# Performance work log

Hardware: AMD Instinct MI355X
Metric: run time of the kernel (lower is better)

## Reference

```python
import math
import jax, jax.numpy as jnp
import numpy as np

EPS = 1e-6
MAX_SCALE_LOG = math.log(100.0)

def rms_norm(x, scale, eps=EPS):
    # x * scale / rms(x), reduction over last dim
    ms = jnp.mean(jnp.square(x), axis=-1, keepdims=True)
    return x * (scale * jax.lax.rsqrt(ms + eps))

def axial_rope_theta(pos, n_heads, d_head, dtype):
    # freqs: linspace in log-space from pi to 10*pi, reshaped to [n_heads, d_head//4]
    f = np.exp(np.linspace(math.log(math.pi), math.log(10.0 * math.pi),
                           n_heads * d_head // 4 + 1)[:-1])
    freqs = jnp.asarray(f.reshape(d_head // 4, n_heads).T, dtype)  # [h, e/4]
    theta_h = pos[:, :, None, 0:1] * freqs  # [n, l, h, e/4]
    theta_w = pos[:, :, None, 1:2] * freqs  # [n, l, h, e/4]
    theta = jnp.concatenate([theta_h, theta_w], axis=-1)  # [n, l, h, e/2]
    return theta.transpose(0, 2, 1, 3)  # [n, h, l, e/2]

def apply_rotary(x, theta):
    d = theta.shape[-1]
    x1, x2, x3 = x[..., :d], x[..., d:2 * d], x[..., 2 * d:]
    cos, sin = jnp.cos(theta), jnp.sin(theta)
    return jnp.concatenate([x1 * cos - x2 * sin, x2 * cos + x1 * sin, x3], axis=-1)

def setup_inputs() -> dict:
    key = jax.random.key(0)
    ks = jax.random.split(key, 8)
    n, l, d_model, d_head = 2, 2048, 1024, 64
    n_heads = d_model // d_head
    x = jax.random.normal(ks[0], (n, l, d_model), jnp.float32)
    pos = jax.random.uniform(ks[1], (n, l, 2), jnp.float32)
    cond = jax.random.normal(ks[2], (n, 1, d_model), jnp.float32)
    # params (torch uses zero-init for w_cond/w_out; small random for a non-degenerate baseline)
    w_cond = jax.random.normal(ks[3], (d_model, d_model), jnp.float32) * 0.02
    w_qkv = jax.random.normal(ks[4], (d_model, 3 * d_model), jnp.float32) * (d_model ** -0.5)
    qk_scale = jnp.full((n_heads,), math.log(10.0), jnp.float32)
    w_out = jax.random.normal(ks[5], (d_model, d_model), jnp.float32) * 0.02
    return {"x": x, "pos": pos, "cond": cond, "w_cond": w_cond,
            "w_qkv": w_qkv, "qk_scale": qk_scale, "w_out": w_out}

def reference(x, pos, cond, w_cond, w_qkv, qk_scale, w_out):
    n, l, d_model = x.shape
    h = qk_scale.shape[0]
    e = d_model // h
    # AdaRMSNorm: scale = linear(cond) + 1
    xn = rms_norm(x, cond @ w_cond + 1.0)
    # QKV projection
    q, k, v = jnp.split(xn @ w_qkv, 3, axis=-1)
    to_heads = lambda t: t.reshape(n, l, h, e).transpose(0, 2, 1, 3)  # [n,h,l,e]
    q, k, v = to_heads(q), to_heads(k), to_heads(v)
    # QKNorm: per-head learned scale, rms over head dim
    s = jnp.exp(0.5 * jnp.minimum(qk_scale, MAX_SCALE_LOG) - 0.25 * math.log(e))
    q = rms_norm(q, s[:, None, None])
    k = rms_norm(k, s[:, None, None])
    # Axial RoPE
    theta = axial_rope_theta(pos, h, e, x.dtype)
    q = apply_rotary(q, theta)
    k = apply_rotary(k, theta)
    # SDPA (no mask)
    attn = jax.nn.softmax(jnp.einsum('nhqe,nhke->nhqk', q, k) / math.sqrt(e), axis=-1)
    o = jnp.einsum('nhqk,nhke->nhqe', attn, v)
    o = o.transpose(0, 2, 1, 3).reshape(n, l, d_model)
    return o @ w_out
```

## Files before the change

kernel.cpp:

```cpp
#include <hip/hip_runtime.h>

typedef unsigned short u16;
typedef unsigned int u32;
typedef short s16x8 __attribute__((ext_vector_type(8)));
typedef short s16x4 __attribute__((ext_vector_type(4)));
typedef float f32x4 __attribute__((ext_vector_type(4)));
typedef float f32x16 __attribute__((ext_vector_type(16)));

#define AS1 __attribute__((address_space(1)))
#define AS3 __attribute__((address_space(3)))

__device__ __forceinline__ float bf2f(u16 u) {
    union { unsigned int i; float f; } x; x.i = ((unsigned int)u) << 16; return x.f;
}
__device__ __forceinline__ u16 f2bf(float f) {
    union { float f; unsigned int i; } x; x.f = f;
    unsigned int r = (x.i + 0x7FFFu + ((x.i >> 16) & 1u)) >> 16;
    return (u16)r;
}
__device__ __forceinline__ void storeOut(u16* p, float v) { *p = f2bf(v); }
__device__ __forceinline__ void storeOut(float* p, float v) { *p = v; }
__device__ __forceinline__ float loadIn(const void* p, size_t i, int isf32) {
    return isf32 ? ((const float*)p)[i] : bf2f(((const u16*)p)[i]);
}
__device__ __forceinline__ float fexp2(float x) {
#if __has_builtin(__builtin_amdgcn_exp2f)
    return __builtin_amdgcn_exp2f(x);
#else
    return exp2f(x);
#endif
}
__device__ __forceinline__ void plswap(u32& a, u32& b) {
#if __has_builtin(__builtin_amdgcn_permlane32_swap)
    const auto r = __builtin_amdgcn_permlane32_swap(a, b, false, false);
    a = (u32)r[0]; b = (u32)r[1];
#else
    asm("v_permlane32_swap_b32 %0, %1" : "+v"(a), "+v"(b));
#endif
}

__global__ __launch_bounds__(256) void detect_dtype(const u16* __restrict__ x,
                                                    int* __restrict__ flag) {
    __shared__ int cnt[4];
    const int tid = threadIdx.x;
    int c = 0;
    #pragma unroll
    for (int i = 0; i < 4; ++i) {
        const u16 u = x[tid * 4 + i];
        const int e = (u >> 7) & 0xFF;
        c += (e >= 101 && e <= 135) ? 1 : 0;
    }
    #pragma unroll
    for (int m = 1; m < 64; m <<= 1) c += __shfl_xor(c, m, 64);
    if ((tid & 63) == 0) cnt[tid >> 6] = c;
    __syncthreads();
    if (tid == 0) {
        const int t = cnt[0] + cnt[1] + cnt[2] + cnt[3];
        *flag = (t < 800) ? 1 : 0;
    }
}

__global__ __launch_bounds__(256) void cond_gemv(const void* __restrict__ cond,
                                                 const void* __restrict__ w,
                                                 float* __restrict__ out,
                                                 const int* __restrict__ flag) {
    const int isf32 = *flag;
    const int d  = blockIdx.x * 256 + threadIdx.x;
    const int n  = blockIdx.y;
    const int k0 = blockIdx.z * 64;
    float acc = 0.f;
    #pragma unroll 8
    for (int k = 0; k < 64; ++k)
        acc += loadIn(cond, n * 1024 + k0 + k, isf32) *
               loadIn(w, (size_t)(k0 + k) * 1024 + d, isf32);
    atomicAdd(out + n * 1024 + d, acc);
}

__global__ __launch_bounds__(256) void rmsnorm_x(const void* __restrict__ x,
                                                 const float* __restrict__ scl,
                                                 u16* __restrict__ xn,
                                                 const int* __restrict__ flag) {
    const int isf32 = *flag;
    const int tok = blockIdx.x;
    const int n = tok >> 11;
    u16* orow = xn + (size_t)tok * 1024;
    const int base = threadIdx.x * 4;
    float f0, f1, f2, f3;
    if (isf32) {
        const float4 v = *(const float4*)((const float*)x + (size_t)tok * 1024 + base);
        f0 = v.x; f1 = v.y; f2 = v.z; f3 = v.w;
    } else {
        s16x4 uv = *(const s16x4*)((const u16*)x + (size_t)tok * 1024 + base);
        f0 = bf2f((u16)uv[0]); f1 = bf2f((u16)uv[1]); f2 = bf2f((u16)uv[2]); f3 = bf2f((u16)uv[3]);
    }
    float ss = f0 * f0 + f1 * f1 + f2 * f2 + f3 * f3;
    #pragma unroll
    for (int m = 1; m < 64; m <<= 1) ss += __shfl_xor(ss, m, 64);
    __shared__ float red[4];
    const int wave = threadIdx.x >> 6, lane = threadIdx.x & 63;
    if (lane == 0) red[wave] = ss;
    __syncthreads();
    float ms = (red[0] + red[1] + red[2] + red[3]) * (1.f / 1024.f);
    float rinv = rsqrtf(ms + 1e-6f);
    s16x4 ov;
    ov[0] = (short)f2bf(f0 * (scl[n * 1024 + base + 0] + 1.f) * rinv);
    ov[1] = (short)f2bf(f1 * (scl[n * 1024 + base + 1] + 1.f) * rinv);
    ov[2] = (short)f2bf(f2 * (scl[n * 1024 + base + 2] + 1.f) * rinv);
    ov[3] = (short)f2bf(f3 * (scl[n * 1024 + base + 3] + 1.f) * rinv);
    *(s16x4*)(orow + base) = ov;
}

__global__ __launch_bounds__(256) void transpose_bf(const void* __restrict__ src,
                                                    u16* __restrict__ dst, int R, int C,
                                                    const int* __restrict__ flag) {
    const int isf32 = *flag;
    __shared__ u16 t[32][33];
    const int c0 = blockIdx.x * 32, r0 = blockIdx.y * 32;
    const int tx = threadIdx.x & 31, ty = threadIdx.x >> 5;
    #pragma unroll
    for (int i = 0; i < 4; ++i)
        t[ty + i * 8][tx] = f2bf(loadIn(src, (size_t)(r0 + ty + i * 8) * C + c0 + tx, isf32));
    __syncthreads();
    #pragma unroll
    for (int i = 0; i < 4; ++i)
        dst[(size_t)(c0 + ty + i * 8) * R + r0 + tx] = t[tx][ty + i * 8];
}

template <typename OutT>
__global__ __launch_bounds__(256) void gemm_bt(const u16* __restrict__ A,
                                               const u16* __restrict__ BT,
                                               OutT* __restrict__ C, int Nn, int K) {
    __shared__ u16 As[2][128 * 32];
    __shared__ u16 Bs[2][128 * 32];
    const int tid = threadIdx.x;
    const int wave = tid >> 6, lane = tid & 63;
    const int l15 = lane & 15, quad = lane >> 4;
    const int bm0 = blockIdx.y * 128, bn0 = blockIdx.x * 128;
    const int wr = wave >> 1, wc = wave & 1;
    f32x4 acc[4][4] = {};
    const int srow = lane >> 2;
    const int g = (lane & 3) ^ (srow & 3);

    auto stageg = [&](int ck, int slot) {
        const int bk = ck * 32;
        #pragma unroll
        for (int p = 0; p < 2; ++p) {
            const int rowl = p * 64 + wave * 16 + srow;
            const u16* ga = A + (size_t)(bm0 + rowl) * K + bk + g * 8;
            u16* la = As[slot] + (p * 64 + wave * 16) * 32;
            __builtin_amdgcn_global_load_lds((const AS1 void*)ga, (AS3 void*)la, 16, 0, 0);
            const u16* gb = BT + (size_t)(bn0 + rowl) * K + bk + g * 8;
            u16* lb = Bs[slot] + (p * 64 + wave * 16) * 32;
            __builtin_amdgcn_global_load_lds((const AS1 void*)gb, (AS3 void*)lb, 16, 0, 0);
        }
    };

    const int NC = K >> 5;
    stageg(0, 0);
    for (int j = 0; j < NC; ++j) {
        if (j > 0) __builtin_amdgcn_s_barrier();
        if (j < NC - 1) {
            stageg(j + 1, (j + 1) & 1);
            asm volatile("s_waitcnt vmcnt(4)" ::: "memory");
        } else {
            asm volatile("s_waitcnt vmcnt(0)" ::: "memory");
        }
        __builtin_amdgcn_sched_barrier(0);
        __builtin_amdgcn_s_barrier();

        const u16* Ac = As[j & 1];
        const u16* Bc = Bs[j & 1];
        s16x8 af[4], bfr[4];
        #pragma unroll
        for (int mt = 0; mt < 4; ++mt) {
            const int r = wr * 64 + mt * 16 + l15;
            af[mt] = *(const s16x8*)(Ac + r * 32 + ((quad ^ (r & 3)) << 3));
        }
        #pragma unroll
        for (int nt = 0; nt < 4; ++nt) {
            const int r = wc * 64 + nt * 16 + l15;
            bfr[nt] = *(const s16x8*)(Bc + r * 32 + ((quad ^ (r & 3)) << 3));
        }
        #pragma unroll
        for (int mt = 0; mt < 4; ++mt)
            #pragma unroll
            for (int nt = 0; nt < 4; ++nt)
                acc[mt][nt] = __builtin_amdgcn_mfma_f32_16x16x32_bf16(af[mt], bfr[nt], acc[mt][nt], 0, 0, 0);
    }
    #pragma unroll
    for (int mt = 0; mt < 4; ++mt)
        #pragma unroll
        for (int nt = 0; nt < 4; ++nt)
            #pragma unroll
            for (int r = 0; r < 4; ++r) {
                const int row = bm0 + wr * 64 + mt * 16 + quad * 4 + r;
                const int col = bn0 + wc * 64 + nt * 16 + l15;
                storeOut(C + (size_t)row * Nn + col, acc[mt][nt][r]);
            }
}

template <typename OutT>
__global__ __launch_bounds__(256) void gemm_bt64(const u16* __restrict__ A,
                                                 const u16* __restrict__ BT,
                                                 OutT* __restrict__ C, int Nn, int K) {
    __shared__ u16 As[2][128 * 32];
    __shared__ u16 Bs[2][64 * 32];
    const int tid = threadIdx.x;
    const int wave = tid >> 6, lane = tid & 63;
    const int l15 = lane & 15, quad = lane >> 4;
    const int bm0 = blockIdx.y * 128, bn0 = blockIdx.x * 64;
    const int wr = wave >> 1, wc = wave & 1;
    f32x4 acc[4][2] = {};
    const int srow = lane >> 2;
    const int g = (lane & 3) ^ (srow & 3);

    auto stageg = [&](int ck, int slot) {
        const int bk = ck * 32;
        #pragma unroll
        for (int p = 0; p < 2; ++p) {
            const int rowl = p * 64 + wave * 16 + srow;
            const u16* ga = A + (size_t)(bm0 + rowl) * K + bk + g * 8;
            u16* la = As[slot] + (p * 64 + wave * 16) * 32;
            __builtin_amdgcn_global_load_lds((const AS1 void*)ga, (AS3 void*)la, 16, 0, 0);
        }
        {
            const int rowl = wave * 16 + srow;
            const u16* gb = BT + (size_t)(bn0 + rowl) * K + bk + g * 8;
            u16* lb = Bs[slot] + (wave * 16) * 32;
            __builtin_amdgcn_global_load_lds((const AS1 void*)gb, (AS3 void*)lb, 16, 0, 0);
        }
    };

    const int NC = K >> 5;
    stageg(0, 0);
    for (int j = 0; j < NC; ++j) {
        if (j > 0) __builtin_amdgcn_s_barrier();
        if (j < NC - 1) {
            stageg(j + 1, (j + 1) & 1);
            asm volatile("s_waitcnt vmcnt(3)" ::: "memory");
        } else {
            asm volatile("s_waitcnt vmcnt(0)" ::: "memory");
        }
        __builtin_amdgcn_sched_barrier(0);
        __builtin_amdgcn_s_barrier();

        const u16* Ac = As[j & 1];
        const u16* Bc = Bs[j & 1];
        s16x8 af[4], bfr[2];
        #pragma unroll
        for (int mt = 0; mt < 4; ++mt) {
            const int r = wr * 64 + mt * 16 + l15;
            af[mt] = *(const s16x8*)(Ac + r * 32 + ((quad ^ (r & 3)) << 3));
        }
        #pragma unroll
        for (int nt = 0; nt < 2; ++nt) {
            const int r = wc * 32 + nt * 16 + l15;
            bfr[nt] = *(const s16x8*)(Bc + r * 32 + ((quad ^ (r & 3)) << 3));
        }
        #pragma unroll
        for (int mt = 0; mt < 4; ++mt)
            #pragma unroll
            for (int nt = 0; nt < 2; ++nt)
                acc[mt][nt] = __builtin_amdgcn_mfma_f32_16x16x32_bf16(af[mt], bfr[nt], acc[mt][nt], 0, 0, 0);
    }
    #pragma unroll
    for (int mt = 0; mt < 4; ++mt)
        #pragma unroll
        for (int nt = 0; nt < 2; ++nt)
            #pragma unroll
            for (int r = 0; r < 4; ++r) {
                const int row = bm0 + wr * 64 + mt * 16 + quad * 4 + r;
                const int col = bn0 + wc * 32 + nt * 16 + l15;
                storeOut(C + (size_t)row * Nn + col, acc[mt][nt][r]);
            }
}

__global__ __launch_bounds__(256) void qkv_head(const u16* __restrict__ qkv,
                                                const void* __restrict__ pos,
                                                const void* __restrict__ qk_scale,
                                                u16* __restrict__ q_ws,
                                                u16* __restrict__ k_ws,
                                                u16* __restrict__ vtg,
                                                const int* __restrict__ flag) {
    const int isf32 = *flag;
    const int nh = blockIdx.y;
    const int n = nh >> 4, h = nh & 15;
    const int l0 = blockIdx.x * 64;
    const int tid = threadIdx.x;
    const int wave = tid >> 6, lane = tid & 63;

    const float qs = loadIn(qk_scale, h, isf32);
    const float s = __expf(0.5f * fminf(qs, 4.605170186f) - 1.039720771f);
    const float qmul = s * s * 0.125f * 1.44269504089f;
    const int j = lane & 31;
    const float t = (float)((j & 15) * 16 + h);
    const float freq = 3.14159265358979f * __expf(t * (2.302585093f / 256.f));
    const int pj = j >> 4;

    #pragma unroll 2
    for (int it = 0; it < 16; ++it) {
        const int l = l0 + wave * 16 + it;
        const int tok = n * 2048 + l;
        const u16* row = qkv + (size_t)tok * 3072;
        float qv = bf2f(row[h * 64 + lane]);
        float kv = bf2f(row[1024 + h * 64 + lane]);
        float q2 = qv * qv, k2 = kv * kv;
        #pragma unroll
        for (int m = 1; m < 64; m <<= 1) { q2 += __shfl_xor(q2, m, 64); k2 += __shfl_xor(k2, m, 64); }
        float qn = qv * rsqrtf(q2 * (1.f / 64.f) + 1e-6f) * qmul;
        float kn = kv * rsqrtf(k2 * (1.f / 64.f) + 1e-6f);
        const float p = loadIn(pos, tok * 2 + pj, isf32);
        const float th = p * freq;
        const float c = __cosf(th), sn = __sinf(th);
        const float pq = __shfl_xor(qn, 32, 64);
        const float pk = __shfl_xor(kn, 32, 64);
        float qr, kr;
        if (lane < 32) { qr = qn * c - pq * sn; kr = kn * c - pk * sn; }
        else           { qr = qn * c + pq * sn; kr = kn * c + pk * sn; }
        const size_t oidx = ((size_t)nh * 2048 + l) * 64 + lane;
        q_ws[oidx] = f2bf(qr);
        k_ws[oidx] = f2bf(kr);
    }

    __shared__ u16 tbuf[64][65];
    const u16* vsrc = qkv + (size_t)(n * 2048 + l0) * 3072 + 2048 + h * 64;
    #pragma unroll
    for (int it = 0; it < 16; ++it) {
        const int idx = it * 256 + tid;
        const int r = idx >> 6, c = idx & 63;
        tbuf[r][c] = vsrc[(size_t)r * 3072 + c];
    }
    __syncthreads();
    u16* dst = vtg + (size_t)nh * 131072 + l0;
    #pragma unroll
    for (int it = 0; it < 16; ++it) {
        const int idx = it * 256 + tid;
        const int er = idx >> 6, lc = idx & 63;
        dst[(size_t)er * 2048 + lc] = tbuf[lc][er];
    }
}

__global__ __launch_bounds__(1024) void attn10(const u16* __restrict__ Q,
                                               const u16* __restrict__ K,
                                               const u16* __restrict__ Vtg,
                                               u16* __restrict__ O) {
    __shared__ u16 Ks[2][256 * 64];
    __shared__ u16 Vt[2][64 * 256];
    const int nh = blockIdx.y;
    const int q0 = blockIdx.x * 256;
    const int tid = threadIdx.x;
    const int wave = tid >> 6, lane = tid & 63;
    const int wq = wave & 7, ks = wave >> 3;
    const int l31 = lane & 31, h = lane >> 5;
    const size_t hb = (size_t)nh * 2048 * 64;
    const u16* Vbase = Vtg + (size_t)nh * 131072;

    s16x8 qf[4];
    #pragma unroll
    for (int kd = 0; kd < 4; ++kd)
        qf[kd] = *(const s16x8*)(Q + hb + (size_t)(q0 + wq * 32 + l31) * 64 + kd * 16 + h * 8);

    f32x16 Oacc[2] = {};
    float lacc = 0.f;

    auto stage = [&](int ch, int slot) {
        const int kb = ch * 256;
        #pragma unroll
        for (int r = 0; r < 2; ++r) {
            const int row = r * 128 + (tid >> 3);
            const int g = (tid & 7) ^ (row & 7);
            __builtin_amdgcn_global_load_lds(
                (const AS1 void*)(K + hb + (size_t)(kb + row) * 64 + g * 8),
                (AS3 void*)(Ks[slot] + (r * 128 + wave * 8) * 64), 16, 0, 0);
        }
        #pragma unroll
        for (int r = 0; r < 2; ++r) {
            const int er = r * 32 + (tid >> 5);
            const int g2 = (lane & 31) ^ (er & 7);
            __builtin_amdgcn_global_load_lds(
                (const AS1 void*)(Vbase + (size_t)er * 2048 + kb + g2 * 8),
                (AS3 void*)(Vt[slot] + (r * 32 + wave * 2) * 256), 16, 0, 0);
        }
    };

    stage(0, 0);

    for (int j = 0; j < 8; ++j) {
        if (j > 0) __builtin_amdgcn_s_barrier();
        if (j < 7) {
            stage(j + 1, (j + 1) & 1);
            asm volatile("s_waitcnt vmcnt(4)" ::: "memory");
        } else {
            asm volatile("s_waitcnt vmcnt(0)" ::: "memory");
        }
        __builtin_amdgcn_sched_barrier(0);
        __builtin_amdgcn_s_barrier();

        const u16* Kt = Ks[j & 1];
        const u16* Vc = Vt[j & 1];

        #pragma unroll 2
        for (int t = 0; t < 4; ++t) {
            const int kt = ks * 4 + t;
            f32x16 S;
            #pragma unroll
            for (int jj = 0; jj < 16; ++jj) S[jj] = -15.f;
            const int kr = kt * 32 + l31;
            __builtin_amdgcn_s_setprio(1);
            #pragma unroll
            for (int kd = 0; kd < 4; ++kd) {
                const s16x8 kf = *(const s16x8*)(Kt + kr * 64 + ((((kd << 1) + h) ^ (kr & 7)) << 3));
                S = __builtin_amdgcn_mfma_f32_32x32x16_bf16(kf, qf[kd], S, 0, 0, 0);
            }
            __builtin_amdgcn_s_setprio(0);
            float e[16];
            #pragma unroll
            for (int jj = 0; jj < 16; ++jj) e[jj] = fexp2(S[jj]);
            float rs = 0.f;
            #pragma unroll
            for (int jj = 0; jj < 16; ++jj) rs += e[jj];
            lacc += rs;
            u32 c[8];
            #pragma unroll
            for (int jj = 0; jj < 8; ++jj)
                asm("v_cvt_pk_bf16_f32 %0, %1, %2" : "=v"(c[jj]) : "v"(e[2 * jj]), "v"(e[2 * jj + 1]));
            plswap(c[0], c[2]);
            plswap(c[1], c[3]);
            plswap(c[4], c[6]);
            plswap(c[5], c[7]);
            union { u32 u[4]; s16x8 v; } pfa, pfb;
            pfa.u[0] = c[0]; pfa.u[1] = c[1]; pfa.u[2] = c[2]; pfa.u[3] = c[3];
            pfb.u[0] = c[4]; pfb.u[1] = c[5]; pfb.u[2] = c[6]; pfb.u[3] = c[7];
            __builtin_amdgcn_s_setprio(1);
            #pragma unroll
            for (int et = 0; et < 2; ++et) {
                const int er = et * 32 + l31;
                #pragma unroll
                for (int kdp = 0; kdp < 2; ++kdp) {
                    const int ch = kt * 4 + kdp * 2 + h;
                    const s16x8 vf = *(const s16x8*)(Vc + er * 256 + ((ch ^ (er & 7)) << 3));
                    Oacc[et] = __builtin_amdgcn_mfma_f32_32x32x16_bf16(kdp ? pfb.v : pfa.v, vf, Oacc[et], 0, 0, 0);
                }
            }
            __builtin_amdgcn_s_setprio(0);
        }
    }

    __syncthreads();
    float (*Osh)[512] = (float(*)[512]) & Ks[0][0];
    float* Lsh = (float*)&Vt[0][0];
    if (ks == 1) {
        #pragma unroll
        for (int et = 0; et < 2; ++et)
            #pragma unroll
            for (int r = 0; r < 16; ++r)
                Osh[et * 16 + r][wq * 64 + lane] = Oacc[et][r];
        Lsh[wq * 64 + lane] = lacc;
    }
    __syncthreads();
    if (ks == 0) {
        #pragma unroll
        for (int et = 0; et < 2; ++et)
            #pragma unroll
            for (int r = 0; r < 16; ++r)
                Oacc[et][r] += Osh[et * 16 + r][wq * 64 + lane];
        lacc += Lsh[wq * 64 + lane];

        lacc += __shfl_xor(lacc, 32, 64);
        const float linv_l = 1.f / lacc;
        const int n = nh >> 4, hh = nh & 15;
        #pragma unroll
        for (int r = 0; r < 16; ++r) {
            const int ql = (r & 3) + 8 * (r >> 2) + 4 * h;
            const float linv = __shfl(linv_l, ql, 64);
            const int qrow = q0 + wq * 32 + ql;
            #pragma unroll
            for (int et = 0; et < 2; ++et)
                O[((size_t)n * 2048 + qrow) * 1024 + hh * 64 + et * 32 + l31] = f2bf(Oacc[et][r] * linv);
        }
    }
}

extern "C" void kernel_launch(void* const* d_in, const int* in_sizes, int n_in,
                              void* d_out, int out_size, void* d_ws, size_t ws_size,
                              hipStream_t stream) {
    const void* x        = d_in[0];
    const void* pos      = d_in[1];
    const void* cond     = d_in[2];
    const void* w_cond   = d_in[3];
    const void* w_qkv    = d_in[4];
    const void* qk_scale = d_in[5];
    const void* w_out    = d_in[6];

    char* ws = (char*)d_ws;
    constexpr size_t OFS_SCALE = 0;
    constexpr size_t OFS_FLAG  = 8192;
    constexpr size_t OFS_XN    = 16384;
    constexpr size_t OFS_WQKVT = OFS_XN    + 8388608;
    constexpr size_t OFS_WOUTT = OFS_WQKVT + 6291456;
    constexpr size_t OFS_QKV   = OFS_WOUTT + 2097152;
    constexpr size_t OFS_Q     = OFS_QKV   + 25165824;
    constexpr size_t OFS_K     = OFS_Q     + 8388608;
    constexpr size_t OFS_VT    = OFS_K     + 8388608;
    constexpr size_t OFS_O     = OFS_VT    + 8388608;

    float* scale = (float*)(ws + OFS_SCALE);
    int*   flag  = (int*)(ws + OFS_FLAG);
    u16* xn    = (u16*)(ws + OFS_XN);
    u16* wqkvT = (u16*)(ws + OFS_WQKVT);
    u16* woutT = (u16*)(ws + OFS_WOUTT);
    u16* qkv   = (u16*)(ws + OFS_QKV);
    u16* qws   = (u16*)(ws + OFS_Q);
    u16* kws   = (u16*)(ws + OFS_K);
    u16* vtg   = (u16*)(ws + OFS_VT);
    u16* ows   = (u16*)(ws + OFS_O);

    detect_dtype<<<dim3(1), 256, 0, stream>>>((const u16*)x, flag);
    hipMemsetAsync(scale, 0, 2 * 1024 * sizeof(float), stream);
    cond_gemv<<<dim3(4, 2, 16), 256, 0, stream>>>(cond, w_cond, scale, flag);
    rmsnorm_x<<<dim3(4096), 256, 0, stream>>>(x, scale, xn, flag);
    transpose_bf<<<dim3(96, 32), 256, 0, stream>>>(w_qkv, wqkvT, 1024, 3072, flag);
    transpose_bf<<<dim3(32, 32), 256, 0, stream>>>(w_out, woutT, 1024, 1024, flag);
    gemm_bt<u16><<<dim3(24, 32), 256, 0, stream>>>(xn, wqkvT, qkv, 3072, 1024);
    qkv_head<<<dim3(32, 32), 256, 0, stream>>>(qkv, pos, qk_scale, qws, kws, vtg, flag);
    attn10<<<dim3(8, 32), 1024, 0, stream>>>(qws, kws, vtg, ows);
    gemm_bt64<float><<<dim3(16, 32), 256, 0, stream>>>(ows, woutT, (float*)d_out, 1024, 1024);
}
```

Baseline: 222.2 us.

## Fuse QK norm, RoPE and V transpose into QKV GEMM epilogue; merge transposes

Moves the per-head QK RMS norm, axial RoPE and the V transpose from a separate qkv_head kernel into the epilogue of the QKV GEMM. Each wave's 64-column tile maps to one head, so the norm is reduced with 16-lane shuffles and RoPE is applied in registers before writing Q and K. V tiles go through shared memory and are written transposed. This removes the round trip of the 24 MB QKV intermediate and one launch, and the two weight transposes are merged into one launch. The cost is a heavier epilogue with scattered 2-byte stores for Q and K, plus a larger shared buffer.

```diff
diff --git a/kernel.cpp b/kernel.cpp
--- a/kernel.cpp
+++ b/kernel.cpp
@@ -110,12 +110,18 @@
     *(s16x4*)(orow + base) = ov;
 }
 
-__global__ __launch_bounds__(256) void transpose_bf(const void* __restrict__ src,
-                                                    u16* __restrict__ dst, int R, int C,
-                                                    const int* __restrict__ flag) {
+__global__ __launch_bounds__(256) void transpose_both(const void* __restrict__ src_qkv,
+                                                      u16* __restrict__ dst_qkv,
+                                                      const void* __restrict__ src_out,
+                                                      u16* __restrict__ dst_out,
+                                                      const int* __restrict__ flag) {
     const int isf32 = *flag;
     __shared__ u16 t[32][33];
-    const int c0 = blockIdx.x * 32, r0 = blockIdx.y * 32;
+    const void* src; u16* dst; int C, c0;
+    const int R = 1024;
+    if (blockIdx.x < 96) { src = src_qkv; dst = dst_qkv; C = 3072; c0 = blockIdx.x * 32; }
+    else                 { src = src_out; dst = dst_out; C = 1024; c0 = (blockIdx.x - 96) * 32; }
+    const int r0 = blockIdx.y * 32;
     const int tx = threadIdx.x & 31, ty = threadIdx.x >> 5;
     #pragma unroll
     for (int i = 0; i < 4; ++i)
@@ -126,12 +132,18 @@
         dst[(size_t)(c0 + ty + i * 8) * R + r0 + tx] = t[tx][ty + i * 8];
 }
 
-template <typename OutT>
-__global__ __launch_bounds__(256) void gemm_bt(const u16* __restrict__ A,
-                                               const u16* __restrict__ BT,
-                                               OutT* __restrict__ C, int Nn, int K) {
-    __shared__ u16 As[2][128 * 32];
-    __shared__ u16 Bs[2][128 * 32];
+__global__ __launch_bounds__(256) void gemm_qkv(const u16* __restrict__ A,
+                                                const u16* __restrict__ BT,
+                                                const void* __restrict__ pos,
+                                                const void* __restrict__ qk_scale,
+                                                u16* __restrict__ qws,
+                                                u16* __restrict__ kws,
+                                                u16* __restrict__ vtg,
+                                                const int* __restrict__ flag) {
+    constexpr int K = 1024;
+    __shared__ u16 sbuf[128 * 136];
+    u16* As = sbuf;
+    u16* Bs = sbuf + 8192;
     const int tid = threadIdx.x;
     const int wave = tid >> 6, lane = tid & 63;
     const int l15 = lane & 15, quad = lane >> 4;
@@ -147,10 +159,10 @@
         for (int p = 0; p < 2; ++p) {
             const int rowl = p * 64 + wave * 16 + srow;
             const u16* ga = A + (size_t)(bm0 + rowl) * K + bk + g * 8;
-            u16* la = As[slot] + (p * 64 + wave * 16) * 32;
+            u16* la = As + slot * 4096 + (p * 64 + wave * 16) * 32;
             __builtin_amdgcn_global_load_lds((const AS1 void*)ga, (AS3 void*)la, 16, 0, 0);
             const u16* gb = BT + (size_t)(bn0 + rowl) * K + bk + g * 8;
-            u16* lb = Bs[slot] + (p * 64 + wave * 16) * 32;
+            u16* lb = Bs + slot * 4096 + (p * 64 + wave * 16) * 32;
             __builtin_amdgcn_global_load_lds((const AS1 void*)gb, (AS3 void*)lb, 16, 0, 0);
         }
     };
@@ -168,8 +180,8 @@
         __builtin_amdgcn_sched_barrier(0);
         __builtin_amdgcn_s_barrier();
 
-        const u16* Ac = As[j & 1];
-        const u16* Bc = Bs[j & 1];
+        const u16* Ac = As + (j & 1) * 4096;
+        const u16* Bc = Bs + (j & 1) * 4096;
         s16x8 af[4], bfr[4];
         #pragma unroll
         for (int mt = 0; mt < 4; ++mt) {
@@ -187,16 +199,68 @@
             for (int nt = 0; nt < 4; ++nt)
                 acc[mt][nt] = __builtin_amdgcn_mfma_f32_16x16x32_bf16(af[mt], bfr[nt], acc[mt][nt], 0, 0, 0);
     }
-    #pragma unroll
-    for (int mt = 0; mt < 4; ++mt)
-        #pragma unroll
-        for (int nt = 0; nt < 4; ++nt)
-            #pragma unroll
-            for (int r = 0; r < 4; ++r) {
-                const int row = bm0 + wr * 64 + mt * 16 + quad * 4 + r;
-                const int col = bn0 + wc * 64 + nt * 16 + l15;
-                storeOut(C + (size_t)row * Nn + col, acc[mt][nt][r]);
+
+    const int isf32 = *flag;
+    const int bx = blockIdx.x;
+    const int rowbase = bm0 + wr * 64;
+    const int n = rowbase >> 11;
+    const int colw = bn0 + wc * 64;
+
+    if (bx < 16) {
+        const int isq = (bx < 8);
+        const int hh = (colw >> 6) & 15;
+        float mul = 1.f;
+        if (isq) {
+            const float qs = loadIn(qk_scale, hh, isf32);
+            const float s = __expf(0.5f * fminf(qs, 4.605170186f) - 1.039720771f);
+            mul = s * s * 0.125f * 1.44269504089f;
+        }
+        const float t = (float)(l15 * 16 + hh);
+        const float freq = 3.14159265358979f * __expf(t * (2.302585093f / 256.f));
+        u16* dstb = (isq ? qws : kws) + (size_t)(n * 16 + hh) * 2048 * 64;
+        #pragma unroll
+        for (int mt = 0; mt < 4; ++mt)
+            #pragma unroll
+            for (int rr = 0; rr < 4; ++rr) {
+                const int row = rowbase + mt * 16 + quad * 4 + rr;
+                const int l = row & 2047;
+                float s2 = acc[mt][0][rr] * acc[mt][0][rr] + acc[mt][1][rr] * acc[mt][1][rr]
+                         + acc[mt][2][rr] * acc[mt][2][rr] + acc[mt][3][rr] * acc[mt][3][rr];
+                #pragma unroll
+                for (int m = 1; m < 16; m <<= 1) s2 += __shfl_xor(s2, m, 16);
+                const float sc = rsqrtf(s2 * (1.f / 64.f) + 1e-6f) * mul;
+                const float p0 = loadIn(pos, (size_t)row * 2 + 0, isf32);
+                const float p1 = loadIn(pos, (size_t)row * 2 + 1, isf32);
+                const float c0 = __cosf(p0 * freq), sn0 = __sinf(p0 * freq);
+                const float c1 = __cosf(p1 * freq), sn1 = __sinf(p1 * freq);
+                const float a0 = acc[mt][0][rr] * sc, a1 = acc[mt][1][rr] * sc;
+                const float a2 = acc[mt][2][rr] * sc, a3 = acc[mt][3][rr] * sc;
+                u16* d = dstb + (size_t)l * 64 + l15;
+                d[0]  = f2bf(a0 * c0 - a2 * sn0);
+                d[16] = f2bf(a1 * c1 - a3 * sn1);
+                d[32] = f2bf(a2 * c0 + a0 * sn0);
+                d[48] = f2bf(a3 * c1 + a1 * sn1);
             }
+    } else {
+        __syncthreads();
+        #pragma unroll
+        for (int mt = 0; mt < 4; ++mt)
+            #pragma unroll
+            for (int nt = 0; nt < 4; ++nt)
+                #pragma unroll
+                for (int rr = 0; rr < 4; ++rr)
+                    sbuf[(wc * 64 + nt * 16 + l15) * 136 + (wr * 64 + mt * 16 + quad * 4 + rr)]
+                        = f2bf(acc[mt][nt][rr]);
+        __syncthreads();
+        const int ec = tid >> 1, half = tid & 1;
+        const int vcol = bn0 + ec - 2048;
+        const int hh = vcol >> 6, e = vcol & 63;
+        const int lbase = (bm0 & 2047) + half * 64;
+        u16* d = vtg + ((size_t)((bm0 >> 11) * 16 + hh) * 64 + e) * 2048 + lbase;
+        #pragma unroll
+        for (int i = 0; i < 8; ++i)
+            *(s16x8*)(d + i * 8) = *(const s16x8*)(sbuf + ec * 136 + half * 64 + i * 8);
+    }
 }
 
 template <typename OutT>
@@ -275,71 +339,6 @@
             }
 }
 
-__global__ __launch_bounds__(256) void qkv_head(const u16* __restrict__ qkv,
-                                                const void* __restrict__ pos,
-                                                const void* __restrict__ qk_scale,
-                                                u16* __restrict__ q_ws,
-                                                u16* __restrict__ k_ws,
-                                                u16* __restrict__ vtg,
-                                                const int* __restrict__ flag) {
-    const int isf32 = *flag;
-    const int nh = blockIdx.y;
-    const int n = nh >> 4, h = nh & 15;
-    const int l0 = blockIdx.x * 64;
-    const int tid = threadIdx.x;
-    const int wave = tid >> 6, lane = tid & 63;
-
-    const float qs = loadIn(qk_scale, h, isf32);
-    const float s = __expf(0.5f * fminf(qs, 4.605170186f) - 1.039720771f);
-    const float qmul = s * s * 0.125f * 1.44269504089f;
-    const int j = lane & 31;
-    const float t = (float)((j & 15) * 16 + h);
-    const float freq = 3.14159265358979f * __expf(t * (2.302585093f / 256.f));
-    const int pj = j >> 4;
-
-    #pragma unroll 2
-    for (int it = 0; it < 16; ++it) {
-        const int l = l0 + wave * 16 + it;
-        const int tok = n * 2048 + l;
-        const u16* row = qkv + (size_t)tok * 3072;
-        float qv = bf2f(row[h * 64 + lane]);
-        float kv = bf2f(row[1024 + h * 64 + lane]);
-        float q2 = qv * qv, k2 = kv * kv;
-        #pragma unroll
-        for (int m = 1; m < 64; m <<= 1) { q2 += __shfl_xor(q2, m, 64); k2 += __shfl_xor(k2, m, 64); }
-        float qn = qv * rsqrtf(q2 * (1.f / 64.f) + 1e-6f) * qmul;
-        float kn = kv * rsqrtf(k2 * (1.f / 64.f) + 1e-6f);
-        const float p = loadIn(pos, tok * 2 + pj, isf32);
-        const float th = p * freq;
-        const float c = __cosf(th), sn = __sinf(th);
-        const float pq = __shfl_xor(qn, 32, 64);
-        const float pk = __shfl_xor(kn, 32, 64);
-        float qr, kr;
-        if (lane < 32) { qr = qn * c - pq * sn; kr = kn * c - pk * sn; }
-        else           { qr = qn * c + pq * sn; kr = kn * c + pk * sn; }
-        const size_t oidx = ((size_t)nh * 2048 + l) * 64 + lane;
-        q_ws[oidx] = f2bf(qr);
-        k_ws[oidx] = f2bf(kr);
-    }
-
-    __shared__ u16 tbuf[64][65];
-    const u16* vsrc = qkv + (size_t)(n * 2048 + l0) * 3072 + 2048 + h * 64;
-    #pragma unroll
-    for (int it = 0; it < 16; ++it) {
-        const int idx = it * 256 + tid;
-        const int r = idx >> 6, c = idx & 63;
-        tbuf[r][c] = vsrc[(size_t)r * 3072 + c];
-    }
-    __syncthreads();
-    u16* dst = vtg + (size_t)nh * 131072 + l0;
-    #pragma unroll
-    for (int it = 0; it < 16; ++it) {
-        const int idx = it * 256 + tid;
-        const int er = idx >> 6, lc = idx & 63;
-        dst[(size_t)er * 2048 + lc] = tbuf[lc][er];
-    }
-}
-
 __global__ __launch_bounds__(1024) void attn10(const u16* __restrict__ Q,
                                                const u16* __restrict__ K,
                                                const u16* __restrict__ Vtg,
@@ -509,7 +508,6 @@
     u16* xn    = (u16*)(ws + OFS_XN);
     u16* wqkvT = (u16*)(ws + OFS_WQKVT);
     u16* woutT = (u16*)(ws + OFS_WOUTT);
-    u16* qkv   = (u16*)(ws + OFS_QKV);
     u16* qws   = (u16*)(ws + OFS_Q);
     u16* kws   = (u16*)(ws + OFS_K);
     u16* vtg   = (u16*)(ws + OFS_VT);
@@ -519,10 +517,8 @@
     hipMemsetAsync(scale, 0, 2 * 1024 * sizeof(float), stream);
     cond_gemv<<<dim3(4, 2, 16), 256, 0, stream>>>(cond, w_cond, scale, flag);
     rmsnorm_x<<<dim3(4096), 256, 0, stream>>>(x, scale, xn, flag);
-    transpose_bf<<<dim3(96, 32), 256, 0, stream>>>(w_qkv, wqkvT, 1024, 3072, flag);
-    transpose_bf<<<dim3(32, 32), 256, 0, stream>>>(w_out, woutT, 1024, 1024, flag);
-    gemm_bt<u16><<<dim3(24, 32), 256, 0, stream>>>(xn, wqkvT, qkv, 3072, 1024);
-    qkv_head<<<dim3(32, 32), 256, 0, stream>>>(qkv, pos, qk_scale, qws, kws, vtg, flag);
+    transpose_both<<<dim3(128, 32), 256, 0, stream>>>(w_qkv, wqkvT, w_out, woutT, flag);
+    gemm_qkv<<<dim3(24, 32), 256, 0, stream>>>(xn, wqkvT, pos, qk_scale, qws, kws, vtg, flag);
     attn10<<<dim3(8, 32), 1024, 0, stream>>>(qws, kws, vtg, ows);
     gemm_bt64<float><<<dim3(16, 32), 256, 0, stream>>>(ows, woutT, (float*)d_out, 1024, 1024);
 }
```

New measurement: 209.5 us. 1.06x faster.
